# Performance work log

Measured on AMD Instinct MI355X. Metric: run time of the kernel, lower is better.

## Reference

```python
import jax, jax.numpy as jnp
import numpy as np

D = 768      # hidden_dim
H = 12       # num_heads
DH = D // H  # head_dim = 64
L = 12       # num_layers
V = 50257    # vocab_size
M = 16       # mini_batch_size (TTT chunk)
LR = 1.0     # ttt_learning_rate
EPS = 1e-5
ROPE_BASE = 10000.0


def _ln(x, w, b):
    mu = jnp.mean(x, axis=-1, keepdims=True)
    var = jnp.mean((x - mu) ** 2, axis=-1, keepdims=True)
    return (x - mu) / jnp.sqrt(var + EPS) * w + b


def _rope(x):
    # x: (B, H, S, DH)
    S, dh = x.shape[2], x.shape[3]
    half = dh // 2
    freqs = 1.0 / (ROPE_BASE ** (jnp.arange(half, dtype=x.dtype) / half))
    ang = jnp.arange(S, dtype=x.dtype)[:, None] * freqs[None, :]  # (S, half)
    cos, sin = jnp.cos(ang), jnp.sin(ang)
    x1, x2 = x[..., :half], x[..., half:]
    return jnp.concatenate([x1 * cos - x2 * sin, x1 * sin + x2 * cos], axis=-1)


def setup_inputs() -> dict:
    key = jax.random.key(0)
    ks = jax.random.split(key, 12)
    std = 0.02
    B, S = 4, 1024
    inp = {
        "input_ids": jax.random.randint(ks[0], (B, S), 0, V),
        "tok_emb": jax.random.normal(ks[1], (V, D), jnp.float32) * std,
        "emb_ln_w": jnp.ones((D,), jnp.float32),
        "emb_ln_b": jnp.zeros((D,), jnp.float32),
        "wq": jax.random.normal(ks[2], (L, D, D), jnp.float32) * std,
        "wk": jax.random.normal(ks[3], (L, D, D), jnp.float32) * std,
        "wv": jax.random.normal(ks[4], (L, D, D), jnp.float32) * std,
        "wo": jax.random.normal(ks[5], (L, D, D), jnp.float32) * std,
        "n1w": jnp.ones((L, D), jnp.float32),
        "n1b": jnp.zeros((L, D), jnp.float32),
        "n2w": jnp.ones((L, D), jnp.float32),
        "n2b": jnp.zeros((L, D), jnp.float32),
        "m1w": jax.random.normal(ks[6], (L, D, 4 * D), jnp.float32) * std,
        "m1b": jnp.zeros((L, 4 * D), jnp.float32),
        "m2w": jax.random.normal(ks[7], (L, 4 * D, D), jnp.float32) * std,
        "m2b": jnp.zeros((L, D), jnp.float32),
        "onw": jnp.ones((D,), jnp.float32),
        "onb": jnp.zeros((D,), jnp.float32),
    }
    return inp


def _forward(input_ids, tok_emb, emb_ln_w, emb_ln_b, wq, wk, wv, wo,
             n1w, n1b, n2w, n2b, m1w, m1b, m2w, m2b, onw, onb):
    B, S = input_ids.shape
    nc = S // M
    eta = LR / M
    mask = jnp.tril(jnp.ones((M, M), tok_emb.dtype))

    x = tok_emb[input_ids]                      # (B, S, D) token embedding
    x = _ln(x, emb_ln_w, emb_ln_b)

    def layer(x, p):
        (lwq, lwk, lwv, lwo, ln1w, ln1b, ln2w, ln2b,
         lm1w, lm1b, lm2w, lm2b) = p
        h = _ln(x, ln1w, ln1b)

        def proj(w):
            return (h @ w).reshape(B, S, H, DH).transpose(0, 2, 1, 3)  # (B,H,S,DH)

        q, k, v = proj(lwq), proj(lwk), proj(lwv)
        q, k = _rope(q), _rope(k)

        def chunks(t):  # (B,H,S,DH) -> (nc,B,H,M,DH)
            return t.reshape(B, H, nc, M, DH).transpose(2, 0, 1, 3, 4)

        qc, kc, vc = chunks(q), chunks(k), chunks(v)
        W0 = jnp.zeros((B, H, DH, DH), x.dtype)  # fast-weight state per head

        def step(W, c):
            qm, km, vm = c                                   # (B,H,M,DH)
            # reconstruction error of current fast weights on this chunk
            E = jnp.einsum('bhmd,bhde->bhme', km, W) - vm    # (B,H,M,DH)
            # causal intra-chunk correction (dual form of per-token GD)
            A = jnp.einsum('bhmd,bhnd->bhmn', qm, km) * mask
            O = (jnp.einsum('bhmd,bhde->bhme', qm, W)
                 - eta * jnp.einsum('bhmn,bhne->bhme', A, E))
            Wn = W - eta * jnp.einsum('bhmd,bhme->bhde', km, E)
            return Wn, O

        _, O = jax.lax.scan(step, W0, (qc, kc, vc))          # (nc,B,H,M,DH)
        o = O.transpose(1, 2, 0, 3, 4).reshape(B, H, S, DH)
        o = o.transpose(0, 2, 1, 3).reshape(B, S, D)
        x = x + o @ lwo

        h2 = _ln(x, ln2w, ln2b)
        x = x + jax.nn.gelu(h2 @ lm1w + lm1b) @ lm2w + lm2b
        return x, None

    x, _ = jax.lax.scan(layer, x,
                        (wq, wk, wv, wo, n1w, n1b, n2w, n2b,
                         m1w, m1b, m2w, m2b))
    x = _ln(x, onw, onb)
    logits = x @ tok_emb.T                                    # tied LM head
    return logits


def reference(input_ids, tok_emb, emb_ln_w, emb_ln_b, wq, wk, wv, wo,
              n1w, n1b, n2w, n2b, m1w, m1b, m2w, m2b, onw, onb):
    return _forward(input_ids, tok_emb, emb_ln_w, emb_ln_b, wq, wk, wv, wo,
                    n1w, n1b, n2w, n2b, m1w, m1b, m2w, m2b, onw, onb)
```

## Files before the change

kernel.cpp:

```cpp
#include <hip/hip_runtime.h>
#include <cstdint>
#include <cstddef>

#define Dm 768
#define Hh 12
#define DHd 64
#define Ll 12
#define Vv 50257
#define Vp 50304
#define Tt 4096
#define Ff 3072
#define QS 2304
#define ETA (1.0f/16.0f)

typedef __attribute__((ext_vector_type(8))) _Float16 half8;
typedef __attribute__((ext_vector_type(8))) unsigned short ushort8;
typedef __attribute__((ext_vector_type(4))) float f32x4;

static __device__ __forceinline__ unsigned short f2h(float f){
  union { _Float16 h; unsigned short u; } c; c.h = (_Float16)f; return c.u;
}
static __device__ __forceinline__ void gload16(const void* g, void* l){
  __builtin_amdgcn_global_load_lds((const __attribute__((address_space(1))) unsigned int*)g,
                                   (__attribute__((address_space(3))) unsigned int*)l, 16, 0, 0);
}
static __device__ __forceinline__ size_t pan_off(int ks, size_t M, int row, int k){
  return ((size_t)ks*M + row)*128 + (size_t)(((k*2) ^ ((row & 7) << 4)));
}

__global__ __launch_bounds__(256)
void convwt_kernel(const float* __restrict__ src, unsigned short* __restrict__ dst,
                   int K, int Ns, int Nd, int coff)
{
  const int l  = blockIdx.y;
  const int nb = blockIdx.x % (Ns/64);
  const int ks = blockIdx.x / (Ns/64);
  const int t  = threadIdx.x;
  __shared__ float tile[64][65];
  const float* W = src + (size_t)l*K*Ns;
  {
    const int r = t >> 2, c0 = (t & 3) * 16;
    const float* s = W + (size_t)(ks*64 + r)*Ns + nb*64 + c0;
    #pragma unroll
    for (int i = 0; i < 4; ++i) {
      const float4 f = *(const float4*)(s + i*4);
      tile[r][c0+i*4+0]=f.x; tile[r][c0+i*4+1]=f.y; tile[r][c0+i*4+2]=f.z; tile[r][c0+i*4+3]=f.w;
    }
  }
  __syncthreads();
  const int n   = t >> 2;
  const int kk0 = (t & 3) * 16;
  const int gn  = coff + nb*64 + n;
  unsigned short bh[16];
  #pragma unroll
  for (int i = 0; i < 16; ++i) bh[i] = f2h(tile[kk0 + i][n]);
  const size_t rowb = ((size_t)l*K*Nd + ((size_t)ks*Nd + gn)*64) * 2;
  const int swz = (gn & 7) << 4;
  char* bD = (char*)dst + rowb;
  *(ushort8*)(bD + ((kk0*2)      ^ swz)) = *(ushort8*)&bh[0];
  *(ushort8*)(bD + ((kk0*2 + 16) ^ swz)) = *(ushort8*)&bh[8];
}

__global__ __launch_bounds__(256)
void convtok_kernel(const float* __restrict__ src, unsigned short* __restrict__ dst)
{
  const int total = 12 * Vp * 8;
  for (int gi = blockIdx.x*256 + threadIdx.x; gi < total; gi += gridDim.x*256) {
    const int j  = gi & 7;
    const int v  = (gi >> 3) % Vp;
    const int ks = gi / (8 * Vp);
    ushort8 u;
    if (v < Vv) {
      const float* s = src + (size_t)v*Dm + ks*64 + j*8;
      const float4 f0 = *(const float4*)s, f1 = *(const float4*)(s+4);
      u[0]=f2h(f0.x); u[1]=f2h(f0.y); u[2]=f2h(f0.z); u[3]=f2h(f0.w);
      u[4]=f2h(f1.x); u[5]=f2h(f1.y); u[6]=f2h(f1.z); u[7]=f2h(f1.w);
    } else {
      #pragma unroll
      for (int q = 0; q < 8; ++q) u[q] = 0;
    }
    const size_t rowb = ((size_t)ks*Vp + v) * 128;
    *(ushort8*)((char*)dst + rowb + ((j*16) ^ ((v&7)<<4))) = u;
  }
}

__global__ __launch_bounds__(256)
void rtab_kernel(float* __restrict__ rt)
{
  const int idx = blockIdx.x*256 + threadIdx.x;
  if (idx >= 1024*64) return;
  const int s = idx >> 6, c = idx & 63, d = c & 31;
  const float freq = powf(10000.0f, -(float)d * (1.0f/32.0f));
  const float ang  = (float)s * freq;
  rt[idx] = (c < 32) ? cosf(ang) : sinf(ang);
}

template<int OMODE>
__global__ __launch_bounds__(256)
void ln_kernel(const float* __restrict__ in, const int* __restrict__ ids,
               const float* __restrict__ w, const float* __restrict__ b,
               void* __restrict__ o1)
{
  const int row = blockIdx.x;
  const int t = threadIdx.x;
  const float* px = in + (ids ? (size_t)ids[row] * Dm : (size_t)row * Dm);
  float x0 = px[t], x1 = px[t+256], x2 = px[t+512];
  float s  = x0 + x1 + x2;
  float s2 = x0*x0 + x1*x1 + x2*x2;
  #pragma unroll
  for (int o = 32; o > 0; o >>= 1) { s += __shfl_xor(s, o); s2 += __shfl_xor(s2, o); }
  __shared__ float ls[4], ls2[4];
  if ((t & 63) == 0) { ls[t>>6] = s; ls2[t>>6] = s2; }
  __syncthreads();
  s  = ls[0]+ls[1]+ls[2]+ls[3];
  s2 = ls2[0]+ls2[1]+ls2[2]+ls2[3];
  const float mu  = s * (1.0f/Dm);
  const float var = s2 * (1.0f/Dm) - mu*mu;
  const float rs  = rsqrtf(var + 1e-5f);
  #pragma unroll
  for (int i = 0; i < 3; ++i) {
    const int c = t + i*256;
    const float xv = (i==0) ? x0 : (i==1) ? x1 : x2;
    const float vv_ = (xv-mu)*rs*w[c] + b[c];
    if (OMODE == 0) {
      ((float*)o1)[(size_t)row * Dm + c] = vv_;
    } else {
      *(unsigned short*)((char*)o1 + pan_off(c >> 6, Tt, row, c & 63)) = f2h(vv_);
    }
  }
}

static __device__ __forceinline__ float4 rot4(float4 a, float4 p, float4 rc, float4 rs, bool hi){
  float4 o;
  if (hi) { o.x = p.x*rs.x + a.x*rc.x; o.y = p.y*rs.y + a.y*rc.y;
            o.z = p.z*rs.z + a.z*rc.z; o.w = p.w*rs.w + a.w*rc.w; }
  else    { o.x = a.x*rc.x - p.x*rs.x; o.y = a.y*rc.y - p.y*rs.y;
            o.z = a.z*rc.z - p.z*rs.z; o.w = a.w*rc.w - p.w*rs.w; }
  return o;
}

__global__ __launch_bounds__(256)
void ttt_scan_kernel(const float* __restrict__ qkv, const float* __restrict__ rt,
                     unsigned short* __restrict__ ob)
{
  const int head = blockIdx.x >> 2;
  const int es   = blockIdx.x & 3;
  const int b  = head / Hh;
  const int hd = head % Hh;
  const int t  = threadIdx.x;
  __shared__ float Wm[64][17];
  __shared__ float kms[16][68];
  __shared__ float qms[16][68];
  __shared__ float Es[16][16];
  __shared__ float Asc[16][16];

  const int e   = t & 15;
  const int m16 = t >> 4;
  const int sr  = t >> 4;
  const int sc  = (t & 15) * 4;
  const bool hi = (sc >= 32);

  for (int i = t; i < 64*17; i += 256) ((float*)Wm)[i] = 0.0f;

  const int tb0 = b * 1024;
  const size_t gbase = (size_t)hd * DHd;

  float4 krR, qrR;
  {
    const size_t ro = (size_t)(tb0 + sr)*QS + gbase;
    const float4 kr = *(const float4*)&qkv[ro + Dm + sc];
    const float4 kp = *(const float4*)&qkv[ro + Dm + (sc^32)];
    const float4 qr = *(const float4*)&qkv[ro + sc];
    const float4 qp = *(const float4*)&qkv[ro + (sc^32)];
    const int s0 = sr;
    const float4 rc = *(const float4*)&rt[s0*64 + (sc&31)];
    const float4 rs = *(const float4*)&rt[s0*64 + 32 + (sc&31)];
    krR = rot4(kr, kp, rc, rs, hi);
    qrR = rot4(qr, qp, rc, rs, hi);
  }
  __syncthreads();

  for (int c = 0; c < 64; ++c) {
    const int tb = tb0 + c*16;
    *(float4*)&kms[sr][sc] = krR;
    *(float4*)&qms[sr][sc] = qrR;
    __syncthreads();
    if (c < 63) {
      const size_t ro = (size_t)(tb + 16 + sr)*QS + gbase;
      const float4 kr = *(const float4*)&qkv[ro + Dm + sc];
      const float4 kp = *(const float4*)&qkv[ro + Dm + (sc^32)];
      const float4 qr = *(const float4*)&qkv[ro + sc];
      const float4 qp = *(const float4*)&qkv[ro + (sc^32)];
      const int sN = (c+1)*16 + sr;
      const float4 rc = *(const float4*)&rt[sN*64 + (sc&31)];
      const float4 rs = *(const float4*)&rt[sN*64 + 32 + (sc&31)];
      krR = rot4(kr, kp, rc, rs, hi);
      qrR = rot4(qr, qp, rc, rs, hi);
    }
    const float vreg = qkv[(size_t)(tb+m16)*QS + 2*Dm + gbase + es*16 + e];
    float aE = -vreg, aO = 0.0f;
    #pragma unroll
    for (int d = 0; d < 64; ++d) {
      const float w_ = Wm[d][e];
      aE += kms[m16][d] * w_;
      aO += qms[m16][d] * w_;
    }
    float aA = 0.0f;
    #pragma unroll
    for (int d = 0; d < 64; ++d) aA += qms[m16][d] * kms[e][d];
    Es[m16][e]  = aE;
    Asc[m16][e] = (e <= m16) ? (-ETA * aA) : 0.0f;
    __syncthreads();
    float acc = aO;
    #pragma unroll
    for (int n = 0; n < 16; ++n) acc += Asc[m16][n] * Es[n][e];
    *(unsigned short*)((char*)ob + pan_off(hd, Tt, tb + m16, es*16 + e)) = f2h(acc);
    #pragma unroll
    for (int j = 0; j < 4; ++j) {
      const int d = m16*4 + j;
      float a = 0.0f;
      #pragma unroll
      for (int m = 0; m < 16; ++m) a += kms[m][d] * Es[m][e];
      Wm[d][e] -= ETA * a;
    }
    __syncthreads();
  }
}

static __device__ __forceinline__ float gelu_f(float x){
  const float u = 0.7978845608028654f * (x + 0.044715f * x*x*x);
  return 0.5f * x * (1.0f + tanhf(u));
}

template<int TM, int TN, bool BIAS, bool GELU_, bool RES, int OUT>
__global__ __launch_bounds__(256)
void gemm_kernel(const unsigned short* __restrict__ A, const unsigned short* __restrict__ B,
                 const float* __restrict__ bias, const float* __restrict__ res,
                 void* __restrict__ o1, int M, int N, int K)
{
  constexpr int FM = TM / 32;
  constexpr int FN = TN / 32;
  __shared__ __attribute__((aligned(16))) unsigned short As[TM*64];
  __shared__ __attribute__((aligned(16))) unsigned short Bs[TN*64];
  const int t    = threadIdx.x;
  const int lane = t & 63;
  const int fr   = lane & 15;
  const int fg   = lane >> 4;
  const int wave = t >> 6;
  const int wm   = (wave >> 1) * (TM/2);
  const int wn   = (wave & 1) * (TN/2);
  const int row0 = blockIdx.y * TM;
  const int n0   = blockIdx.x * TN;

  f32x4 acc[FM][FN];
  #pragma unroll
  for (int i = 0; i < FM; ++i)
    #pragma unroll
    for (int j = 0; j < FN; ++j)
      #pragma unroll
      for (int r = 0; r < 4; ++r) acc[i][j][r] = 0.0f;

  for (int ks = 0; ks*64 < K; ++ks) {
    {
      const char* gB = (const char*)B + ((size_t)ks*N + n0) * 128;
      #pragma unroll
      for (int r = 0; r < TN/32; ++r) {
        const int chunk = (r*4 + wave) * 1024;
        gload16(gB + chunk + lane*16, (char*)Bs + chunk);
      }
    }
    {
      const char* gA = (const char*)A + ((size_t)ks*M + row0) * 128;
      #pragma unroll
      for (int r = 0; r < TM/32; ++r) {
        const int chunk = (r*4 + wave) * 1024;
        gload16(gA + chunk + lane*16, (char*)As + chunk);
      }
    }
    __syncthreads();
    #pragma unroll
    for (int kh = 0; kh < 2; ++kh) {
      half8 af[FM], bf[FN];
      const int swz = (fr & 7) << 4;
      #pragma unroll
      for (int mt = 0; mt < FM; ++mt)
        af[mt] = *(const half8*)((const char*)As + (((wm + mt*16 + fr)*128 + kh*64 + fg*16) ^ swz));
      #pragma unroll
      for (int nt = 0; nt < FN; ++nt)
        bf[nt] = *(const half8*)((const char*)Bs + (((wn + nt*16 + fr)*128 + kh*64 + fg*16) ^ swz));
      #pragma unroll
      for (int mt = 0; mt < FM; ++mt)
        #pragma unroll
        for (int nt = 0; nt < FN; ++nt)
          acc[mt][nt] = __builtin_amdgcn_mfma_f32_16x16x32_f16(af[mt], bf[nt], acc[mt][nt], 0, 0, 0);
    }
    __syncthreads();
  }

  #pragma unroll
  for (int mt = 0; mt < FM; ++mt) {
    #pragma unroll
    for (int nt = 0; nt < FN; ++nt) {
      const int col = n0 + wn + nt*16 + fr;
      const int rbase = row0 + wm + mt*16 + fg*4;
      const float bcol = BIAS ? bias[col] : 0.0f;
      #pragma unroll
      for (int r = 0; r < 4; ++r) {
        float val = acc[mt][nt][r];
        if (BIAS)  val += bcol;
        if (GELU_) val = gelu_f(val);
        if (OUT == 1) {
          *(unsigned short*)((char*)o1 + pan_off(col >> 6, M, rbase + r, col & 63)) = f2h(val);
        } else {
          const size_t off = (size_t)(rbase + r) * N + col;
          float v2 = val;
          if (RES) v2 += res[off];
          ((float*)o1)[off] = v2;
        }
      }
    }
  }
}

template<bool PRE>
__global__ __launch_bounds__(256)
void logits_kernel(const unsigned short* __restrict__ hop, const float* __restrict__ tok,
                   const unsigned short* __restrict__ tokb, float* __restrict__ C)
{
  __shared__ __attribute__((aligned(16))) unsigned short As[128*64];
  __shared__ __attribute__((aligned(16))) unsigned short Bs[128*64];
  int bid = blockIdx.x;
  bid = (bid & 7) * 1572 + (bid >> 3);
  const int n0   = (bid >> 5) * 128;
  const int row0 = (bid & 31) * 128;

  const int t    = threadIdx.x;
  const int lane = t & 63;
  const int fr   = lane & 15;
  const int fg   = lane >> 4;
  const int wave = t >> 6;
  const int wm   = (wave >> 1) * 64;
  const int wn   = (wave & 1) * 64;

  const int arow = t >> 1;
  const int ach  = (t & 1) * 32;

  f32x4 acc[4][4];
  #pragma unroll
  for (int i = 0; i < 4; ++i)
    #pragma unroll
    for (int j = 0; j < 4; ++j)
      #pragma unroll
      for (int r = 0; r < 4; ++r) acc[i][j][r] = 0.0f;

  for (int ks = 0; ks < 12; ++ks) {
    {
      const char* gA = (const char*)hop + ((size_t)ks*Tt + row0) * 128;
      #pragma unroll
      for (int p = 0; p < 4; ++p) {
        const int off = p*4096 + t*16;
        const ushort8 u = *(const ushort8*)(gA + off);
        *(ushort8*)((char*)As + off) = u;
      }
    }
    if (PRE) {
      const char* gB = (const char*)tokb + ((size_t)ks*Vp + n0) * 128;
      #pragma unroll
      for (int p = 0; p < 4; ++p) {
        const int off = p*4096 + t*16;
        const ushort8 u = *(const ushort8*)(gB + off);
        *(ushort8*)((char*)Bs + off) = u;
      }
    } else {
      const int brow = n0 + arow;
      if (brow < Vv) {
        const float* src = &tok[(size_t)brow * Dm + ks*64 + ach];
        #pragma unroll
        for (int i = 0; i < 4; ++i) {
          const float4 f0 = *(const float4*)(src + i*8);
          const float4 f1 = *(const float4*)(src + i*8 + 4);
          ushort8 u;
          u[0]=f2h(f0.x); u[1]=f2h(f0.y); u[2]=f2h(f0.z); u[3]=f2h(f0.w);
          u[4]=f2h(f1.x); u[5]=f2h(f1.y); u[6]=f2h(f1.z); u[7]=f2h(f1.w);
          const int byt = (arow*128 + (ach + i*8)*2) ^ ((arow & 7) << 4);
          *(ushort8*)((char*)Bs + byt) = u;
        }
      } else {
        ushort8 z;
        #pragma unroll
        for (int j = 0; j < 8; ++j) z[j] = 0;
        #pragma unroll
        for (int i = 0; i < 4; ++i) {
          const int byt = (arow*128 + (ach + i*8)*2) ^ ((arow & 7) << 4);
          *(ushort8*)((char*)Bs + byt) = z;
        }
      }
    }
    __syncthreads();
    #pragma unroll
    for (int kh = 0; kh < 2; ++kh) {
      half8 af[4], bf[4];
      const int swz = (fr & 7) << 4;
      #pragma unroll
      for (int mt = 0; mt < 4; ++mt)
        af[mt] = *(const half8*)((const char*)As + (((wm + mt*16 + fr)*128 + kh*64 + fg*16) ^ swz));
      #pragma unroll
      for (int nt = 0; nt < 4; ++nt)
        bf[nt] = *(const half8*)((const char*)Bs + (((wn + nt*16 + fr)*128 + kh*64 + fg*16) ^ swz));
      #pragma unroll
      for (int mt = 0; mt < 4; ++mt)
        #pragma unroll
        for (int nt = 0; nt < 4; ++nt)
          acc[mt][nt] = __builtin_amdgcn_mfma_f32_16x16x32_f16(af[mt], bf[nt], acc[mt][nt], 0, 0, 0);
    }
    __syncthreads();
  }

  #pragma unroll
  for (int mt = 0; mt < 4; ++mt) {
    #pragma unroll
    for (int nt = 0; nt < 4; ++nt) {
      const int col = n0 + wn + nt*16 + fr;
      if (col < Vv) {
        const int rbase = row0 + wm + mt*16 + fg*4;
        #pragma unroll
        for (int r = 0; r < 4; ++r)
          C[(size_t)(rbase + r) * Vv + col] = acc[mt][nt][r];
      }
    }
  }
}

extern "C" void kernel_launch(void* const* d_in, const int* in_sizes, int n_in,
                              void* d_out, int out_size, void* d_ws, size_t ws_size,
                              hipStream_t stream)
{
  const int*   ids = (const int*)  d_in[0];
  const float* tok = (const float*)d_in[1];
  const float* ew  = (const float*)d_in[2];
  const float* eb  = (const float*)d_in[3];
  const float* wq  = (const float*)d_in[4];
  const float* wk  = (const float*)d_in[5];
  const float* wv  = (const float*)d_in[6];
  const float* wo  = (const float*)d_in[7];
  const float* n1w = (const float*)d_in[8];
  const float* n1b = (const float*)d_in[9];
  const float* n2w = (const float*)d_in[10];
  const float* n2b = (const float*)d_in[11];
  const float* m1w = (const float*)d_in[12];
  const float* m1b = (const float*)d_in[13];
  const float* m2w = (const float*)d_in[14];
  const float* m2b = (const float*)d_in[15];
  const float* onw = (const float*)d_in[16];
  const float* onb = (const float*)d_in[17];

  const size_t SP = (size_t)12 * Tt * 64;
  float* x = (float*)d_ws;
  unsigned short* hP = (unsigned short*)(x + (size_t)Tt * Dm);
  unsigned short* ho = hP + SP;
  float* rt = (float*)(ho + SP);
  unsigned short* tokb = (unsigned short*)(rt + 1024*64);
  const size_t ws_need = (size_t)Tt*Dm*4 + SP*2*2 + 1024*64*4 + (size_t)12*Vp*64*2;
  const bool pre = (ws_size >= ws_need);

  float* out = (float*)d_out;
  unsigned short* gP  = (unsigned short*)d_out;
  float* qkv = (float*)((char*)d_out + (size_t)28*1024*1024);
  unsigned short* obP = (unsigned short*)((char*)d_out + (size_t)68*1024*1024);
  unsigned short* wbase = (unsigned short*)((char*)d_out + (size_t)80*1024*1024);
  const size_t SQKV = (size_t)Ll * Dm * QS;
  const size_t SWO  = (size_t)Ll * Dm * Dm;
  const size_t SM   = (size_t)Ll * Dm * Ff;
  unsigned short* qkvW = wbase;
  unsigned short* woW  = qkvW + SQKV;
  unsigned short* m1W  = woW  + SWO;
  unsigned short* m2W  = m1W  + SM;

  convwt_kernel<<<dim3(12*12, Ll), 256, 0, stream>>>(wq, qkvW, Dm, Dm, QS, 0);
  convwt_kernel<<<dim3(12*12, Ll), 256, 0, stream>>>(wk, qkvW, Dm, Dm, QS, Dm);
  convwt_kernel<<<dim3(12*12, Ll), 256, 0, stream>>>(wv, qkvW, Dm, Dm, QS, 2*Dm);
  convwt_kernel<<<dim3(12*12, Ll), 256, 0, stream>>>(wo, woW, Dm, Dm, Dm, 0);
  convwt_kernel<<<dim3(12*48, Ll), 256, 0, stream>>>(m1w, m1W, Dm, Ff, Ff, 0);
  convwt_kernel<<<dim3(48*12, Ll), 256, 0, stream>>>(m2w, m2W, Ff, Dm, Dm, 0);
  rtab_kernel<<<256, 256, 0, stream>>>(rt);
  if (pre) convtok_kernel<<<2048, 256, 0, stream>>>(tok, tokb);

  ln_kernel<0><<<Tt, 256, 0, stream>>>(tok, ids, ew, eb, x);

  for (int l = 0; l < Ll; ++l) {
    ln_kernel<1><<<Tt, 256, 0, stream>>>(x, nullptr, n1w + l*Dm, n1b + l*Dm, hP);
    gemm_kernel<128,128,false,false,false,0><<<dim3(QS/128, Tt/128), 256, 0, stream>>>(
        hP, qkvW + (size_t)l*Dm*QS, nullptr, nullptr, qkv, Tt, QS, Dm);
    ttt_scan_kernel<<<192, 256, 0, stream>>>(qkv, rt, obP);
    gemm_kernel<128,64,false,false,true,0><<<dim3(Dm/64, Tt/128), 256, 0, stream>>>(
        obP, woW + (size_t)l*Dm*Dm, nullptr, x, x, Tt, Dm, Dm);
    ln_kernel<1><<<Tt, 256, 0, stream>>>(x, nullptr, n2w + l*Dm, n2b + l*Dm, hP);
    gemm_kernel<128,128,true,true,false,1><<<dim3(Ff/128, Tt/128), 256, 0, stream>>>(
        hP, m1W + (size_t)l*Dm*Ff, m1b + (size_t)l*Ff, nullptr, gP, Tt, Ff, Dm);
    gemm_kernel<128,64,true,false,true,0><<<dim3(Dm/64, Tt/128), 256, 0, stream>>>(
        gP, m2W + (size_t)l*Ff*Dm, m2b + (size_t)l*Dm, x, x, Tt, Dm, Ff);
  }

  ln_kernel<1><<<Tt, 256, 0, stream>>>(x, nullptr, onw, onb, ho);
  if (pre)
    logits_kernel<true><<<dim3(12576, 1), 256, 0, stream>>>(ho, tok, tokb, out);
  else
    logits_kernel<false><<<dim3(12576, 1), 256, 0, stream>>>(ho, tok, nullptr, out);
}
```

Before: 4.373 ms.

## Double-buffer GEMM LDS tiles, store QKV in fp16, async loads in logits

Adds double-buffered LDS staging to the generic GEMM and the logits kernel, so the next K-slice's global-to-LDS loads are issued before the MFMAs on the current slice. The logits kernel also switches from register-staged copies to direct global_load_lds for its A and B tiles. The QKV projection now writes fp16 instead of fp32, and the TTT scan reads it as half, which halves that intermediate's traffic but reduces its precision. LDS use per block doubles, which may lower occupancy.

```diff
diff --git a/kernel.cpp b/kernel.cpp
--- a/kernel.cpp
+++ b/kernel.cpp
@@ -19,6 +19,12 @@
 
 static __device__ __forceinline__ unsigned short f2h(float f){
   union { _Float16 h; unsigned short u; } c; c.h = (_Float16)f; return c.u;
+}
+static __device__ __forceinline__ float h2f(unsigned short u){
+  union { unsigned short u; _Float16 h; } c; c.u = u; return (float)c.h;
+}
+static __device__ __forceinline__ float4 h4(ushort4 u){
+  float4 f; f.x=h2f(u.x); f.y=h2f(u.y); f.z=h2f(u.z); f.w=h2f(u.w); return f;
 }
 static __device__ __forceinline__ void gload16(const void* g, void* l){
   __builtin_amdgcn_global_load_lds((const __attribute__((address_space(1))) unsigned int*)g,
@@ -140,7 +146,7 @@
 }
 
 __global__ __launch_bounds__(256)
-void ttt_scan_kernel(const float* __restrict__ qkv, const float* __restrict__ rt,
+void ttt_scan_kernel(const unsigned short* __restrict__ qkv, const float* __restrict__ rt,
                      unsigned short* __restrict__ ob)
 {
   const int head = blockIdx.x >> 2;
@@ -168,13 +174,12 @@
   float4 krR, qrR;
   {
     const size_t ro = (size_t)(tb0 + sr)*QS + gbase;
-    const float4 kr = *(const float4*)&qkv[ro + Dm + sc];
-    const float4 kp = *(const float4*)&qkv[ro + Dm + (sc^32)];
-    const float4 qr = *(const float4*)&qkv[ro + sc];
-    const float4 qp = *(const float4*)&qkv[ro + (sc^32)];
-    const int s0 = sr;
-    const float4 rc = *(const float4*)&rt[s0*64 + (sc&31)];
-    const float4 rs = *(const float4*)&rt[s0*64 + 32 + (sc&31)];
+    const float4 kr = h4(*(const ushort4*)&qkv[ro + Dm + sc]);
+    const float4 kp = h4(*(const ushort4*)&qkv[ro + Dm + (sc^32)]);
+    const float4 qr = h4(*(const ushort4*)&qkv[ro + sc]);
+    const float4 qp = h4(*(const ushort4*)&qkv[ro + (sc^32)]);
+    const float4 rc = *(const float4*)&rt[sr*64 + (sc&31)];
+    const float4 rs = *(const float4*)&rt[sr*64 + 32 + (sc&31)];
     krR = rot4(kr, kp, rc, rs, hi);
     qrR = rot4(qr, qp, rc, rs, hi);
   }
@@ -187,17 +192,17 @@
     __syncthreads();
     if (c < 63) {
       const size_t ro = (size_t)(tb + 16 + sr)*QS + gbase;
-      const float4 kr = *(const float4*)&qkv[ro + Dm + sc];
-      const float4 kp = *(const float4*)&qkv[ro + Dm + (sc^32)];
-      const float4 qr = *(const float4*)&qkv[ro + sc];
-      const float4 qp = *(const float4*)&qkv[ro + (sc^32)];
+      const float4 kr = h4(*(const ushort4*)&qkv[ro + Dm + sc]);
+      const float4 kp = h4(*(const ushort4*)&qkv[ro + Dm + (sc^32)]);
+      const float4 qr = h4(*(const ushort4*)&qkv[ro + sc]);
+      const float4 qp = h4(*(const ushort4*)&qkv[ro + (sc^32)]);
       const int sN = (c+1)*16 + sr;
       const float4 rc = *(const float4*)&rt[sN*64 + (sc&31)];
       const float4 rs = *(const float4*)&rt[sN*64 + 32 + (sc&31)];
       krR = rot4(kr, kp, rc, rs, hi);
       qrR = rot4(qr, qp, rc, rs, hi);
     }
-    const float vreg = qkv[(size_t)(tb+m16)*QS + 2*Dm + gbase + es*16 + e];
+    const float vreg = h2f(qkv[(size_t)(tb+m16)*QS + 2*Dm + gbase + es*16 + e]);
     float aE = -vreg, aO = 0.0f;
     #pragma unroll
     for (int d = 0; d < 64; ++d) {
@@ -240,8 +245,8 @@
 {
   constexpr int FM = TM / 32;
   constexpr int FN = TN / 32;
-  __shared__ __attribute__((aligned(16))) unsigned short As[TM*64];
-  __shared__ __attribute__((aligned(16))) unsigned short Bs[TN*64];
+  __shared__ __attribute__((aligned(16))) unsigned short As[2][TM*64];
+  __shared__ __attribute__((aligned(16))) unsigned short Bs[2][TN*64];
   const int t    = threadIdx.x;
   const int lane = t & 63;
   const int fr   = lane & 15;
@@ -251,6 +256,7 @@
   const int wn   = (wave & 1) * (TN/2);
   const int row0 = blockIdx.y * TM;
   const int n0   = blockIdx.x * TN;
+  const int NK   = K >> 6;
 
   f32x4 acc[FM][FN];
   #pragma unroll
@@ -260,34 +266,38 @@
       #pragma unroll
       for (int r = 0; r < 4; ++r) acc[i][j][r] = 0.0f;
 
-  for (int ks = 0; ks*64 < K; ++ks) {
-    {
-      const char* gB = (const char*)B + ((size_t)ks*N + n0) * 128;
-      #pragma unroll
-      for (int r = 0; r < TN/32; ++r) {
-        const int chunk = (r*4 + wave) * 1024;
-        gload16(gB + chunk + lane*16, (char*)Bs + chunk);
-      }
-    }
-    {
-      const char* gA = (const char*)A + ((size_t)ks*M + row0) * 128;
-      #pragma unroll
-      for (int r = 0; r < TM/32; ++r) {
-        const int chunk = (r*4 + wave) * 1024;
-        gload16(gA + chunk + lane*16, (char*)As + chunk);
-      }
-    }
-    __syncthreads();
+  auto stage = [&](int bufi, int ks) {
+    const char* gB = (const char*)B + ((size_t)ks*N + n0) * 128;
+    char* lB = (char*)&Bs[bufi][0];
+    #pragma unroll
+    for (int r = 0; r < TN/32; ++r) {
+      const int chunk = (r*4 + wave) * 1024;
+      gload16(gB + chunk + lane*16, lB + chunk);
+    }
+    const char* gA = (const char*)A + ((size_t)ks*M + row0) * 128;
+    char* lA = (char*)&As[bufi][0];
+    #pragma unroll
+    for (int r = 0; r < TM/32; ++r) {
+      const int chunk = (r*4 + wave) * 1024;
+      gload16(gA + chunk + lane*16, lA + chunk);
+    }
+  };
+
+  stage(0, 0);
+  __syncthreads();
+  int cur = 0;
+  for (int ks = 0; ks < NK; ++ks) {
+    if (ks + 1 < NK) stage(cur ^ 1, ks + 1);
     #pragma unroll
     for (int kh = 0; kh < 2; ++kh) {
       half8 af[FM], bf[FN];
       const int swz = (fr & 7) << 4;
       #pragma unroll
       for (int mt = 0; mt < FM; ++mt)
-        af[mt] = *(const half8*)((const char*)As + (((wm + mt*16 + fr)*128 + kh*64 + fg*16) ^ swz));
+        af[mt] = *(const half8*)((const char*)&As[cur][0] + (((wm + mt*16 + fr)*128 + kh*64 + fg*16) ^ swz));
       #pragma unroll
       for (int nt = 0; nt < FN; ++nt)
-        bf[nt] = *(const half8*)((const char*)Bs + (((wn + nt*16 + fr)*128 + kh*64 + fg*16) ^ swz));
+        bf[nt] = *(const half8*)((const char*)&Bs[cur][0] + (((wn + nt*16 + fr)*128 + kh*64 + fg*16) ^ swz));
       #pragma unroll
       for (int mt = 0; mt < FM; ++mt)
         #pragma unroll
@@ -295,6 +305,7 @@
           acc[mt][nt] = __builtin_amdgcn_mfma_f32_16x16x32_f16(af[mt], bf[nt], acc[mt][nt], 0, 0, 0);
     }
     __syncthreads();
+    cur ^= 1;
   }
 
   #pragma unroll
@@ -311,6 +322,8 @@
         if (GELU_) val = gelu_f(val);
         if (OUT == 1) {
           *(unsigned short*)((char*)o1 + pan_off(col >> 6, M, rbase + r, col & 63)) = f2h(val);
+        } else if (OUT == 2) {
+          ((unsigned short*)o1)[(size_t)(rbase + r) * N + col] = f2h(val);
         } else {
           const size_t off = (size_t)(rbase + r) * N + col;
           float v2 = val;
@@ -327,8 +340,8 @@
 void logits_kernel(const unsigned short* __restrict__ hop, const float* __restrict__ tok,
                    const unsigned short* __restrict__ tokb, float* __restrict__ C)
 {
-  __shared__ __attribute__((aligned(16))) unsigned short As[128*64];
-  __shared__ __attribute__((aligned(16))) unsigned short Bs[128*64];
+  __shared__ __attribute__((aligned(16))) unsigned short As[2][128*64];
+  __shared__ __attribute__((aligned(16))) unsigned short Bs[2][128*64];
   int bid = blockIdx.x;
   bid = (bid & 7) * 1572 + (bid >> 3);
   const int n0   = (bid >> 5) * 128;
@@ -341,7 +354,6 @@
   const int wave = t >> 6;
   const int wm   = (wave >> 1) * 64;
   const int wn   = (wave & 1) * 64;
-
   const int arow = t >> 1;
   const int ach  = (t & 1) * 32;
 
@@ -353,23 +365,21 @@
       #pragma unroll
       for (int r = 0; r < 4; ++r) acc[i][j][r] = 0.0f;
 
-  for (int ks = 0; ks < 12; ++ks) {
-    {
-      const char* gA = (const char*)hop + ((size_t)ks*Tt + row0) * 128;
-      #pragma unroll
-      for (int p = 0; p < 4; ++p) {
-        const int off = p*4096 + t*16;
-        const ushort8 u = *(const ushort8*)(gA + off);
-        *(ushort8*)((char*)As + off) = u;
-      }
+  auto stage = [&](int bufi, int ks) {
+    const char* gA = (const char*)hop + ((size_t)ks*Tt + row0) * 128;
+    char* lA = (char*)&As[bufi][0];
+    #pragma unroll
+    for (int r = 0; r < 4; ++r) {
+      const int chunk = (r*4 + wave) * 1024;
+      gload16(gA + chunk + lane*16, lA + chunk);
     }
     if (PRE) {
       const char* gB = (const char*)tokb + ((size_t)ks*Vp + n0) * 128;
-      #pragma unroll
-      for (int p = 0; p < 4; ++p) {
-        const int off = p*4096 + t*16;
-        const ushort8 u = *(const ushort8*)(gB + off);
-        *(ushort8*)((char*)Bs + off) = u;
+      char* lB = (char*)&Bs[bufi][0];
+      #pragma unroll
+      for (int r = 0; r < 4; ++r) {
+        const int chunk = (r*4 + wave) * 1024;
+        gload16(gB + chunk + lane*16, lB + chunk);
       }
     } else {
       const int brow = n0 + arow;
@@ -383,7 +393,7 @@
           u[0]=f2h(f0.x); u[1]=f2h(f0.y); u[2]=f2h(f0.z); u[3]=f2h(f0.w);
           u[4]=f2h(f1.x); u[5]=f2h(f1.y); u[6]=f2h(f1.z); u[7]=f2h(f1.w);
           const int byt = (arow*128 + (ach + i*8)*2) ^ ((arow & 7) << 4);
-          *(ushort8*)((char*)Bs + byt) = u;
+          *(ushort8*)((char*)&Bs[bufi][0] + byt) = u;
         }
       } else {
         ushort8 z;
@@ -392,21 +402,27 @@
         #pragma unroll
         for (int i = 0; i < 4; ++i) {
           const int byt = (arow*128 + (ach + i*8)*2) ^ ((arow & 7) << 4);
-          *(ushort8*)((char*)Bs + byt) = z;
+          *(ushort8*)((char*)&Bs[bufi][0] + byt) = z;
         }
       }
     }
-    __syncthreads();
+  };
+
+  stage(0, 0);
+  __syncthreads();
+  int cur = 0;
+  for (int ks = 0; ks < 12; ++ks) {
+    if (ks + 1 < 12) stage(cur ^ 1, ks + 1);
     #pragma unroll
     for (int kh = 0; kh < 2; ++kh) {
       half8 af[4], bf[4];
       const int swz = (fr & 7) << 4;
       #pragma unroll
       for (int mt = 0; mt < 4; ++mt)
-        af[mt] = *(const half8*)((const char*)As + (((wm + mt*16 + fr)*128 + kh*64 + fg*16) ^ swz));
+        af[mt] = *(const half8*)((const char*)&As[cur][0] + (((wm + mt*16 + fr)*128 + kh*64 + fg*16) ^ swz));
       #pragma unroll
       for (int nt = 0; nt < 4; ++nt)
-        bf[nt] = *(const half8*)((const char*)Bs + (((wn + nt*16 + fr)*128 + kh*64 + fg*16) ^ swz));
+        bf[nt] = *(const half8*)((const char*)&Bs[cur][0] + (((wn + nt*16 + fr)*128 + kh*64 + fg*16) ^ swz));
       #pragma unroll
       for (int mt = 0; mt < 4; ++mt)
         #pragma unroll
@@ -414,6 +430,7 @@
           acc[mt][nt] = __builtin_amdgcn_mfma_f32_16x16x32_f16(af[mt], bf[nt], acc[mt][nt], 0, 0, 0);
     }
     __syncthreads();
+    cur ^= 1;
   }
 
   #pragma unroll
@@ -465,9 +482,9 @@
 
   float* out = (float*)d_out;
   unsigned short* gP  = (unsigned short*)d_out;
-  float* qkv = (float*)((char*)d_out + (size_t)28*1024*1024);
-  unsigned short* obP = (unsigned short*)((char*)d_out + (size_t)68*1024*1024);
-  unsigned short* wbase = (unsigned short*)((char*)d_out + (size_t)80*1024*1024);
+  unsigned short* qkv = (unsigned short*)((char*)d_out + (size_t)28*1024*1024);
+  unsigned short* obP = (unsigned short*)((char*)d_out + (size_t)50*1024*1024);
+  unsigned short* wbase = (unsigned short*)((char*)d_out + (size_t)60*1024*1024);
   const size_t SQKV = (size_t)Ll * Dm * QS;
   const size_t SWO  = (size_t)Ll * Dm * Dm;
   const size_t SM   = (size_t)Ll * Dm * Ff;
@@ -489,7 +506,7 @@
 
   for (int l = 0; l < Ll; ++l) {
     ln_kernel<1><<<Tt, 256, 0, stream>>>(x, nullptr, n1w + l*Dm, n1b + l*Dm, hP);
-    gemm_kernel<128,128,false,false,false,0><<<dim3(QS/128, Tt/128), 256, 0, stream>>>(
+    gemm_kernel<128,128,false,false,false,2><<<dim3(QS/128, Tt/128), 256, 0, stream>>>(
         hP, qkvW + (size_t)l*Dm*QS, nullptr, nullptr, qkv, Tt, QS, Dm);
     ttt_scan_kernel<<<192, 256, 0, stream>>>(qkv, rt, obP);
     gemm_kernel<128,64,false,false,true,0><<<dim3(Dm/64, Tt/128), 256, 0, stream>>>(
```

New measurement: 4.654 ms. 6.4% more time.
